# Kernel tuning notes

Hardware: AMD Instinct MI355X
Metric: run time of the kernel (lower is better)

Reference implementation:

```python
import jax, jax.numpy as jnp
import numpy as np
from jax import lax

LEAK = 0.2   # LeakyReLU negative slope
EPS = 1e-5   # LayerNorm eps (torch default)
K = 16       # nsample

def _lrelu(x):
    return jnp.where(x > 0, x, LEAK * x)

def _ln(x, g, b):
    m = x.mean(-1, keepdims=True)
    v = x.var(-1, keepdims=True)
    return (x - m) / jnp.sqrt(v + EPS) * g + b

def _pointconv(xyz, new_xyz, feats, W, b):
    # xyz [B,N,3], new_xyz [B,M,3], feats [B,N,C] -> [B,M,O]
    d2 = (jnp.sum(new_xyz**2, -1)[:, :, None]
          + jnp.sum(xyz**2, -1)[:, None, :]
          - 2.0 * jnp.einsum('bmd,bnd->bmn', new_xyz, xyz))   # [B,M,N]
    _, idx = lax.top_k(-d2, K)                                # kNN indices [B,M,K]
    bidx = jnp.arange(xyz.shape[0])[:, None, None]
    g_xyz = xyz[bidx, idx] - new_xyz[:, :, None, :]           # relative coords [B,M,K,3]
    g_f = feats[bidx, idx]                                    # neighbor feats  [B,M,K,C]
    g = jnp.concatenate([g_xyz, g_f], -1)                     # [B,M,K,C+3]
    h = _lrelu(jnp.einsum('bmkc,co->bmko', g, W) + b)         # local MLP
    return h.max(2)                                           # max-pool over neighbors

def setup_inputs():
    key = jax.random.key(0)
    ks = jax.random.split(key, 8)
    B, N, base, C1 = 256, 1024, 16, 32
    def w(k, shape, fan):
        return jax.random.normal(k, shape, jnp.float32) * (1.0 / np.sqrt(fan))
    return dict(
        point_cloud=jax.random.normal(ks[0], (B, 3, N), jnp.float32),
        pw_W0=w(ks[1], (3, base), 3), pw_b0=jnp.zeros(base), pw_g0=jnp.ones(base), pw_beta0=jnp.zeros(base),
        pw_W1=w(ks[2], (base, base), base), pw_b1=jnp.zeros(base), pw_g1=jnp.ones(base), pw_beta1=jnp.zeros(base),
        pc0_W=w(ks[3], (base + 3, C1), base + 3), pc0_b=jnp.zeros(C1),
        bn_Ws=w(ks[4], (C1, C1 // 4), C1), bn_bs=jnp.zeros(C1 // 4),
        bn_Wc=w(ks[5], (C1 // 4 + 3, 128), C1 // 4 + 3), bn_bc=jnp.zeros(128),
        bn_We=w(ks[6], (128, 256), 128), bn_be=jnp.zeros(256),
    )

def reference(point_cloud, pw_W0, pw_b0, pw_g0, pw_beta0, pw_W1, pw_b1, pw_g1, pw_beta1,
              pc0_W, pc0_b, bn_Ws, bn_bs, bn_Wc, bn_bc, bn_We, bn_be):
    xyz0 = jnp.swapaxes(point_cloud, 1, 2)   # [B,1024,3]
    xyz1 = xyz0[:, ::2]                      # strided downsample -> [B,512,3]
    xyz2 = xyz1[:, ::4]                      # -> [B,128,3]
    # pointwise MLP (Linear-LN-LeakyReLU x2)
    f = _lrelu(_ln(xyz0 @ pw_W0 + pw_b0, pw_g0, pw_beta0))
    f = _lrelu(_ln(f @ pw_W1 + pw_b1, pw_g1, pw_beta1))       # [B,1024,16]
    # PointConv layer 0: 1024 -> 512 points, 16 -> 32 ch
    f = _pointconv(xyz0, xyz1, f, pc0_W, pc0_b)               # [B,512,32]
    # BottleneckStridedPointConv: squeeze (32->8), grouped conv (->128), expand (->256)
    fs = _lrelu(f @ bn_Ws + bn_bs)                            # [B,512,8]
    f = _pointconv(xyz1, xyz2, fs, bn_Wc, bn_bc)              # [B,128,128]
    f = f @ bn_We + bn_be                                     # [B,128,256]
    return f.mean(1)                                          # mean over points -> [B,256]
```

## Files before the change

kernel.cpp:

```cpp
#include <hip/hip_runtime.h>
#include <float.h>
#include <math.h>

#define LEAK 0.2f
#define EPS 1e-5f

__device__ __forceinline__ float lrelu(float v){ return v > 0.f ? v : LEAK*v; }

__device__ __forceinline__ void ln_lrelu16(float* h, const float* __restrict__ g, const float* __restrict__ be){
  float mu = 0.f;
#pragma unroll
  for (int o=0;o<16;o++) mu += h[o];
  mu *= 0.0625f;
  float var = 0.f;
#pragma unroll
  for (int o=0;o<16;o++){ float d = h[o]-mu; var += d*d; }
  var *= 0.0625f;
  float rs = 1.0f / sqrtf(var + EPS);
#pragma unroll
  for (int o=0;o<16;o++){ float v = (h[o]-mu)*rs*g[o] + be[o]; h[o] = lrelu(v); }
}

__global__ __launch_bounds__(256) void prep_kernel(const float* __restrict__ pc,
    const float* __restrict__ W0, const float* __restrict__ b0, const float* __restrict__ g0, const float* __restrict__ be0,
    const float* __restrict__ W1, const float* __restrict__ b1, const float* __restrict__ g1, const float* __restrict__ be1,
    float4* __restrict__ cand, float* __restrict__ feats)
{
  const int p = blockIdx.x*256 + threadIdx.x;
  const int b = p >> 10, n = p & 1023;
  const float* base = pc + b*3072;
  const float x = base[n], y = base[1024+n], z = base[2048+n];
  cand[p] = make_float4(x, y, z, x*x + y*y + z*z);
  float h[16];
#pragma unroll
  for (int o=0;o<16;o++) h[o] = b0[o] + x*W0[o] + y*W0[16+o] + z*W0[32+o];
  ln_lrelu16(h, g0, be0);
  float h2[16];
#pragma unroll
  for (int o=0;o<16;o++){
    float s = b1[o];
#pragma unroll
    for (int c=0;c<16;c++) s += h[c]*W1[c*16+o];
    h2[o] = s;
  }
  ln_lrelu16(h2, g1, be1);
  float4* fo = (float4*)(feats + p*16);
  fo[0] = make_float4(h2[0],h2[1],h2[2],h2[3]);
  fo[1] = make_float4(h2[4],h2[5],h2[6],h2[7]);
  fo[2] = make_float4(h2[8],h2[9],h2[10],h2[11]);
  fo[3] = make_float4(h2[12],h2[13],h2[14],h2[15]);
}

#define KNN_SENT 0xFF7FFC00u
__device__ __forceinline__ unsigned enc_key(float d, int n){
  unsigned u = __float_as_uint(d);
  u ^= (unsigned)(((int)u) >> 31) | 0x80000000u;
  return (u & ~1023u) | (unsigned)n;
}
__device__ __forceinline__ float dec_key(unsigned k){
  unsigned u = k ^ ((unsigned)(~(((int)k) >> 31)) | 0x80000000u);
  return __uint_as_float(u);
}

__device__ __forceinline__ unsigned med3u(unsigned a, unsigned b, unsigned c){
  unsigned d;
  asm("v_med3_u32 %0, %1, %2, %3" : "=v"(d) : "v"(a), "v"(b), "v"(c));
  return d;
}

__device__ __forceinline__ void ins_sorted(unsigned (&dk)[16], unsigned key){
#pragma unroll
  for (int j=15;j>0;--j) dk[j] = med3u(dk[j-1], dk[j], key);
  dk[0] = key < dk[0] ? key : dk[0];
}

template<int QS, int CS, int NQTOT, int NQ, int SPLIT, int NCAND>
__device__ __forceinline__ void knn_body(unsigned* md, float4* scand,
    const float4* __restrict__ cand, int bid, int* __restrict__ idx_out)
{
  constexpr int NC = NCAND / SPLIT;
  constexpr int QG = NQTOT / NQ;
  constexpr int W  = SPLIT*NQ;
  constexpr int QSL = QS / CS;
  const int b = bid / QG, qg = bid % QG;
  const int tid = threadIdx.x;
  const int m = tid & (NQ-1), s = tid / NQ;
  const int mg = qg*NQ + m;
  const float4* __restrict__ cb = cand + b*1024;

  for (int i = tid; i < NCAND; i += NQ*SPLIT)
    scand[i] = cb[i*CS];
  __syncthreads();

  const float4 qv = scand[mg*QSL];
  const float qx2=-2.f*qv.x, qy2=-2.f*qv.y, qz2=-2.f*qv.z;
  const int n0u = __builtin_amdgcn_readfirstlane(s*NC);

  unsigned dk[16];
#pragma unroll
  for (int j=0;j<16;j++) dk[j] = KNN_SENT;

#pragma unroll 8
  for (int t=0;t<32;t++){
    float4 c = scand[n0u+t];
    float d = fmaf(c.x,qx2, fmaf(c.y,qy2, fmaf(c.z,qz2, c.w)));
    ins_sorted(dk, enc_key(d, n0u+t));
  }
  float Tf = dec_key(dk[15]);

  {
    unsigned m32 = 0u;
#pragma unroll 8
    for (int t=32;t<64;t++){
      float4 c = scand[n0u+t];
      float d = fmaf(c.x,qx2, fmaf(c.y,qy2, fmaf(c.z,qz2, c.w)));
      if (d < Tf) m32 |= (1u<<(t-32));
    }
    while (m32){
      const int t = __builtin_ctz(m32) + 32;
      m32 &= m32-1u;
      float4 c = scand[n0u+t];
      float d = fmaf(c.x,qx2, fmaf(c.y,qy2, fmaf(c.z,qz2, c.w)));
      ins_sorted(dk, enc_key(d, n0u+t));
    }
    Tf = dec_key(dk[15]);
  }

  for (int ch=1; ch<NC/64; ch++){
    const int cb0u = n0u + ch*64;
    unsigned long long msk = 0ull;
#pragma unroll 16
    for (int t=0;t<64;t++){
      float4 c = scand[cb0u+t];
      float d = fmaf(c.x,qx2, fmaf(c.y,qy2, fmaf(c.z,qz2, c.w)));
      if (d < Tf) msk |= (1ull<<t);
    }
    while (msk){
      const int t = __builtin_ctzll(msk);
      msk &= msk-1ull;
      float4 c = scand[cb0u+t];
      float d = fmaf(c.x,qx2, fmaf(c.y,qy2, fmaf(c.z,qz2, c.w)));
      ins_sorted(dk, enc_key(d, cb0u+t));
    }
    Tf = dec_key(dk[15]);
  }

  if constexpr (SPLIT > 1){
    if (s > 0){
      const int col = s*NQ + m;
#pragma unroll
      for (int j=0;j<16;j++) md[j*W + col] = dk[j];
    }
#pragma unroll
    for (int step = SPLIT/2; step > 1; step >>= 1){
      __syncthreads();
      if (s < step){
        const int col2 = (s+step)*NQ + m;
#pragma unroll
        for (int j=0;j<16;j++) ins_sorted(dk, md[j*W + col2]);
        if (s > 0){
          const int col = s*NQ + m;
#pragma unroll
          for (int j=0;j<16;j++) md[j*W + col] = dk[j];
        }
      }
    }
    __syncthreads();
    if (s != 0) return;
    const int col2 = NQ + m;
#pragma unroll
    for (int j=0;j<16;j++){
      unsigned o = md[(15-j)*W + col2];
      dk[j] = o < dk[j] ? o : dk[j];
    }
  }

  int ik[16];
#pragma unroll
  for (int j=0;j<16;j++) ik[j] = (int)(dk[j] & 1023u);
  int4* op = (int4*)(idx_out + (b*NQTOT + mg)*16);
  op[0] = make_int4(ik[0],ik[1],ik[2],ik[3]);
  op[1] = make_int4(ik[4],ik[5],ik[6],ik[7]);
  op[2] = make_int4(ik[8],ik[9],ik[10],ik[11]);
  op[3] = make_int4(ik[12],ik[13],ik[14],ik[15]);
}

__global__ __attribute__((amdgpu_flat_work_group_size(1024,1024), amdgpu_waves_per_eu(4,8)))
void knn_fused_kernel(const float4* __restrict__ cand,
                      int* __restrict__ idx1, int* __restrict__ idx2)
{
  __shared__ __align__(16) char smem[81920];
  unsigned* md = (unsigned*)smem;
  if (blockIdx.x < 256){
    float4* scand = (float4*)(smem + 65536);
    knn_body<2,1,512,512,2,1024>(md, scand, cand, blockIdx.x, idx1);
  } else {
    float4* scand = (float4*)(smem + 65536);
    knn_body<8,2,128,128,8,512>(md, scand, cand, blockIdx.x - 256, idx2);
  }
}

__global__ __attribute__((amdgpu_flat_work_group_size(512,512), amdgpu_waves_per_eu(4,4)))
void feat1_kernel(const float4* __restrict__ cand,
    const float* __restrict__ feats, const int* __restrict__ idx1,
    const float* __restrict__ W, const float* __restrict__ Wb,
    const float* __restrict__ Ws,
    float* __restrict__ p1part)
{
  __shared__ float sPT[16*1024];
  const int bx = blockIdx.x;
  const int b = bx >> 1, ob = bx & 1;
  const int ob16 = ob*16;
  const int tid = threadIdx.x;
  const float4* __restrict__ cb = cand + b*1024;
  const float4* __restrict__ fb4 = (const float4*)(feats + b*16384);

#pragma unroll
  for (int i=0;i<2;i++){
    const int j = tid + i*512;
    float4 cj = cb[j];
    float4 f0 = fb4[j*4+0], f1 = fb4[j*4+1], f2 = fb4[j*4+2], f3 = fb4[j*4+3];
    float f[16] = {f0.x,f0.y,f0.z,f0.w, f1.x,f1.y,f1.z,f1.w,
                   f2.x,f2.y,f2.z,f2.w, f3.x,f3.y,f3.z,f3.w};
#pragma unroll
    for (int o4=0;o4<4;o4++){
      float4 s = *(const float4*)(Wb + ob16 + o4*4);
      { float4 wa = *(const float4*)(W +       ob16 + o4*4);
        float4 wb = *(const float4*)(W + 32  + ob16 + o4*4);
        float4 wc = *(const float4*)(W + 64  + ob16 + o4*4);
        s.x = fmaf(cj.x,wa.x, fmaf(cj.y,wb.x, fmaf(cj.z,wc.x, s.x)));
        s.y = fmaf(cj.x,wa.y, fmaf(cj.y,wb.y, fmaf(cj.z,wc.y, s.y)));
        s.z = fmaf(cj.x,wa.z, fmaf(cj.y,wb.z, fmaf(cj.z,wc.z, s.z)));
        s.w = fmaf(cj.x,wa.w, fmaf(cj.y,wb.w, fmaf(cj.z,wc.w, s.w))); }
#pragma unroll
      for (int c=0;c<16;c++){
        float4 w = *(const float4*)(W + (3+c)*32 + ob16 + o4*4);
        s.x = fmaf(f[c], w.x, s.x);
        s.y = fmaf(f[c], w.y, s.y);
        s.z = fmaf(f[c], w.z, s.z);
        s.w = fmaf(f[c], w.w, s.w);
      }
      sPT[(o4*4+0)*1024 + j] = s.x;
      sPT[(o4*4+1)*1024 + j] = s.y;
      sPT[(o4*4+2)*1024 + j] = s.z;
      sPT[(o4*4+3)*1024 + j] = s.w;
    }
  }
  __syncthreads();

  const int m = tid;
  const float4 qv = cb[2*m];
  float Q[16];
#pragma unroll
  for (int i=0;i<4;i++){
    float4 a = *(const float4*)(W +       ob16 + i*4);
    float4 bb= *(const float4*)(W + 32  + ob16 + i*4);
    float4 cc= *(const float4*)(W + 64  + ob16 + i*4);
    Q[i*4+0] = fmaf(qv.x,a.x, fmaf(qv.y,bb.x, qv.z*cc.x));
    Q[i*4+1] = fmaf(qv.x,a.y, fmaf(qv.y,bb.y, qv.z*cc.y));
    Q[i*4+2] = fmaf(qv.x,a.z, fmaf(qv.y,bb.z, qv.z*cc.z));
    Q[i*4+3] = fmaf(qv.x,a.w, fmaf(qv.y,bb.w, qv.z*cc.w));
  }
  int idxr[16];
  { const int4* ip = (const int4*)(idx1 + (b*512+m)*16);
    int4 a=ip[0], b2=ip[1], c2=ip[2], d2=ip[3];
    idxr[0]=a.x; idxr[1]=a.y; idxr[2]=a.z; idxr[3]=a.w;
    idxr[4]=b2.x; idxr[5]=b2.y; idxr[6]=b2.z; idxr[7]=b2.w;
    idxr[8]=c2.x; idxr[9]=c2.y; idxr[10]=c2.z; idxr[11]=c2.w;
    idxr[12]=d2.x; idxr[13]=d2.y; idxr[14]=d2.z; idxr[15]=d2.w; }

  float acc[16];
#pragma unroll
  for (int o=0;o<16;o++) acc[o] = -FLT_MAX;

#pragma unroll 4
  for (int k=0;k<16;k++){
    const int j = idxr[k];
    const float* pj = sPT + j;
#pragma unroll
    for (int o=0;o<16;o++)
      acc[o] = fmaxf(acc[o], pj[o*1024] - Q[o]);
  }

  float fsacc[8] = {0.f,0.f,0.f,0.f,0.f,0.f,0.f,0.f};
#pragma unroll
  for (int o=0;o<16;o++){
    const float a = fmaxf(acc[o], 0.2f*acc[o]);
    float4 u = *(const float4*)(Ws + (ob16+o)*8);
    float4 v = *(const float4*)(Ws + (ob16+o)*8 + 4);
    fsacc[0] = fmaf(a, u.x, fsacc[0]);
    fsacc[1] = fmaf(a, u.y, fsacc[1]);
    fsacc[2] = fmaf(a, u.z, fsacc[2]);
    fsacc[3] = fmaf(a, u.w, fsacc[3]);
    fsacc[4] = fmaf(a, v.x, fsacc[4]);
    fsacc[5] = fmaf(a, v.y, fsacc[5]);
    fsacc[6] = fmaf(a, v.z, fsacc[6]);
    fsacc[7] = fmaf(a, v.w, fsacc[7]);
  }
  float4* op = (float4*)(p1part + ((b*2+ob)*512 + m)*8);
  op[0] = make_float4(fsacc[0],fsacc[1],fsacc[2],fsacc[3]);
  op[1] = make_float4(fsacc[4],fsacc[5],fsacc[6],fsacc[7]);
}

__global__ __attribute__((amdgpu_flat_work_group_size(512,512), amdgpu_waves_per_eu(4,4)))
void feat2_kernel(const float4* __restrict__ cand,
    const float* __restrict__ p1part, const int* __restrict__ idx2,
    const float* __restrict__ Wc, const float* __restrict__ bc,
    const float* __restrict__ bs,
    float* __restrict__ p2red)
{
  __shared__ float sP2[512*32];
  __shared__ float sred[32];
  const int bx = blockIdx.x;
  const int b = bx >> 2, ob = bx & 3;
  const int o_base = ob*32;
  const int tid = threadIdx.x;
  const float4* __restrict__ cb = cand + b*1024;
  if (tid < 32) sred[tid] = 0.f;

  { const float4* __restrict__ pa4 = (const float4*)(p1part + ((b*2+0)*512 + tid)*8);
    const float4* __restrict__ pb4 = (const float4*)(p1part + ((b*2+1)*512 + tid)*8);
    float4 a0 = pa4[0], a1 = pa4[1], c0 = pb4[0], c1 = pb4[1];
    float4 s0 = *(const float4*)(bs), s1 = *(const float4*)(bs+4);
    float f[8];
    f[0]=lrelu(a0.x+c0.x+s0.x); f[1]=lrelu(a0.y+c0.y+s0.y);
    f[2]=lrelu(a0.z+c0.z+s0.z); f[3]=lrelu(a0.w+c0.w+s0.w);
    f[4]=lrelu(a1.x+c1.x+s1.x); f[5]=lrelu(a1.y+c1.y+s1.y);
    f[6]=lrelu(a1.z+c1.z+s1.z); f[7]=lrelu(a1.w+c1.w+s1.w);
    float4 cj = cb[2*tid];
    float* row = sP2 + tid*32;
    const int sw = (tid & 7);
#pragma unroll
    for (int o4=0;o4<8;o4++){
      float4 s = *(const float4*)(bc + o_base + o4*4);
      { float4 wa = *(const float4*)(Wc +        o_base + o4*4);
        float4 wb = *(const float4*)(Wc + 128  + o_base + o4*4);
        float4 wc = *(const float4*)(Wc + 256  + o_base + o4*4);
        s.x = fmaf(cj.x,wa.x, fmaf(cj.y,wb.x, fmaf(cj.z,wc.x, s.x)));
        s.y = fmaf(cj.x,wa.y, fmaf(cj.y,wb.y, fmaf(cj.z,wc.y, s.y)));
        s.z = fmaf(cj.x,wa.z, fmaf(cj.y,wb.z, fmaf(cj.z,wc.z, s.z)));
        s.w = fmaf(cj.x,wa.w, fmaf(cj.y,wb.w, fmaf(cj.z,wc.w, s.w))); }
#pragma unroll
      for (int c=0;c<8;c++){
        float4 w = *(const float4*)(Wc + (3+c)*128 + o_base + o4*4);
        s.x = fmaf(f[c], w.x, s.x);
        s.y = fmaf(f[c], w.y, s.y);
        s.z = fmaf(f[c], w.z, s.z);
        s.w = fmaf(f[c], w.w, s.w);
      }
      *(float4*)(row + ((o4 ^ sw) << 2)) = s;
    }
  }
  __syncthreads();

  const int m = tid >> 2, oq = tid & 3;
  const float4 qv = cb[8*m];
  float Q[8];
  { const int og = o_base + oq*8;
#pragma unroll
    for (int i=0;i<2;i++){
      float4 a = *(const float4*)(Wc +        og + i*4);
      float4 bb= *(const float4*)(Wc + 128  + og + i*4);
      float4 cc= *(const float4*)(Wc + 256  + og + i*4);
      Q[i*4+0] = fmaf(qv.x,a.x, fmaf(qv.y,bb.x, qv.z*cc.x));
      Q[i*4+1] = fmaf(qv.x,a.y, fmaf(qv.y,bb.y, qv.z*cc.y));
      Q[i*4+2] = fmaf(qv.x,a.z, fmaf(qv.y,bb.z, qv.z*cc.z));
      Q[i*4+3] = fmaf(qv.x,a.w, fmaf(qv.y,bb.w, qv.z*cc.w));
    } }
  int idxr[16];
  { const int4* ip = (const int4*)(idx2 + (b*128+m)*16);
    int4 a=ip[0], b2=ip[1], c2=ip[2], d2=ip[3];
    idxr[0]=a.x; idxr[1]=a.y; idxr[2]=a.z; idxr[3]=a.w;
    idxr[4]=b2.x; idxr[5]=b2.y; idxr[6]=b2.z; idxr[7]=b2.w;
    idxr[8]=c2.x; idxr[9]=c2.y; idxr[10]=c2.z; idxr[11]=c2.w;
    idxr[12]=d2.x; idxr[13]=d2.y; idxr[14]=d2.z; idxr[15]=d2.w; }

  float acc[8];
#pragma unroll
  for (int o=0;o<8;o++) acc[o] = -FLT_MAX;

#pragma unroll 4
  for (int k=0;k<16;k++){
    const int j = idxr[k];
    const float* row = sP2 + j*32;
    const int sw = (j & 7);
    float4 p0 = *(const float4*)(row + (((2*oq  ) ^ sw) << 2));
    float4 p1 = *(const float4*)(row + (((2*oq+1) ^ sw) << 2));
    acc[0] = fmaxf(acc[0], p0.x - Q[0]);
    acc[1] = fmaxf(acc[1], p0.y - Q[1]);
    acc[2] = fmaxf(acc[2], p0.z - Q[2]);
    acc[3] = fmaxf(acc[3], p0.w - Q[3]);
    acc[4] = fmaxf(acc[4], p1.x - Q[4]);
    acc[5] = fmaxf(acc[5], p1.y - Q[5]);
    acc[6] = fmaxf(acc[6], p1.z - Q[6]);
    acc[7] = fmaxf(acc[7], p1.w - Q[7]);
  }

#pragma unroll
  for (int o=0;o<8;o++){
    float v = fmaxf(acc[o], 0.2f*acc[o]);
    v += __shfl_xor(v, 4);
    v += __shfl_xor(v, 8);
    v += __shfl_xor(v, 16);
    v += __shfl_xor(v, 32);
    if ((threadIdx.x & 60) == 0)
      atomicAdd(&sred[oq*8+o], v);
  }
  __syncthreads();
  if (tid < 32) p2red[b*128 + o_base + tid] = sred[tid];
}

__global__ __launch_bounds__(256) void final_kernel(const float* __restrict__ p2red,
    const float* __restrict__ We, const float* __restrict__ beF, float* __restrict__ out)
{
  const int b = blockIdx.x, o = threadIdx.x;
  const float* __restrict__ r0 = p2red + b*128;
  float s = 0.f;
#pragma unroll 8
  for (int c=0;c<128;c++) s += r0[c]*We[c*256+o];
  out[b*256+o] = beF[o] + s*0.0078125f;
}

extern "C" void kernel_launch(void* const* d_in, const int* in_sizes, int n_in,
                              void* d_out, int out_size, void* d_ws, size_t ws_size,
                              hipStream_t stream) {
  (void)in_sizes; (void)n_in; (void)out_size; (void)ws_size;
  const float* pc   = (const float*)d_in[0];
  const float* W0   = (const float*)d_in[1];
  const float* b0   = (const float*)d_in[2];
  const float* g0   = (const float*)d_in[3];
  const float* be0  = (const float*)d_in[4];
  const float* W1   = (const float*)d_in[5];
  const float* b1   = (const float*)d_in[6];
  const float* g1   = (const float*)d_in[7];
  const float* be1  = (const float*)d_in[8];
  const float* pcW  = (const float*)d_in[9];
  const float* pcb  = (const float*)d_in[10];
  const float* Ws   = (const float*)d_in[11];
  const float* bs   = (const float*)d_in[12];
  const float* Wc   = (const float*)d_in[13];
  const float* bc   = (const float*)d_in[14];
  const float* We   = (const float*)d_in[15];
  const float* beF  = (const float*)d_in[16];

  char* ws = (char*)d_ws;
  float4* cand0 = (float4*)ws;
  float*  feats = (float*)(ws + (4u<<20));
  float*  p2red = (float*)(ws + (4u<<20));
  int*    idx1  = (int*)  (ws + (20u<<20));
  int*    idx2  = (int*)  (ws + (28u<<20));
  float*  p1part= (float*)(ws + (30u<<20));
  float*  out   = (float*)d_out;

  prep_kernel<<<1024, 256, 0, stream>>>(pc, W0,b0,g0,be0, W1,b1,g1,be1, cand0, feats);
  knn_fused_kernel<<<512, 1024, 0, stream>>>(cand0, idx1, idx2);
  feat1_kernel<<<512, 512, 0, stream>>>(cand0, feats, idx1, pcW, pcb, Ws, p1part);
  feat2_kernel<<<1024, 512, 0, stream>>>(cand0, p1part, idx2, Wc, bc, bs, p2red);
  final_kernel<<<256, 256, 0, stream>>>(p2red, We, beF, out);
}
```

Before: 211.8 us.

## Fold prep into kNN/feat1 and final GEMV into feat2 via last-block counter

Removes the separate prep kernel. kNN now builds its candidate float4s straight from the raw point cloud, and feat1 recomputes the pointwise MLP and LayerNorm per point instead of reading a stored feature buffer. The final expand-and-mean GEMV moves into feat2, where the last of the four blocks per batch, found through an atomic counter, does the work. This cuts two kernel launches and the cand/feats global round-trips, at the cost of redundant MLP compute in feat1 (done by both output-half blocks), a memset, and release/acquire atomics.

```diff
diff --git a/kernel.cpp b/kernel.cpp
--- a/kernel.cpp
+++ b/kernel.cpp
@@ -19,36 +19,6 @@
   float rs = 1.0f / sqrtf(var + EPS);
 #pragma unroll
   for (int o=0;o<16;o++){ float v = (h[o]-mu)*rs*g[o] + be[o]; h[o] = lrelu(v); }
-}
-
-__global__ __launch_bounds__(256) void prep_kernel(const float* __restrict__ pc,
-    const float* __restrict__ W0, const float* __restrict__ b0, const float* __restrict__ g0, const float* __restrict__ be0,
-    const float* __restrict__ W1, const float* __restrict__ b1, const float* __restrict__ g1, const float* __restrict__ be1,
-    float4* __restrict__ cand, float* __restrict__ feats)
-{
-  const int p = blockIdx.x*256 + threadIdx.x;
-  const int b = p >> 10, n = p & 1023;
-  const float* base = pc + b*3072;
-  const float x = base[n], y = base[1024+n], z = base[2048+n];
-  cand[p] = make_float4(x, y, z, x*x + y*y + z*z);
-  float h[16];
-#pragma unroll
-  for (int o=0;o<16;o++) h[o] = b0[o] + x*W0[o] + y*W0[16+o] + z*W0[32+o];
-  ln_lrelu16(h, g0, be0);
-  float h2[16];
-#pragma unroll
-  for (int o=0;o<16;o++){
-    float s = b1[o];
-#pragma unroll
-    for (int c=0;c<16;c++) s += h[c]*W1[c*16+o];
-    h2[o] = s;
-  }
-  ln_lrelu16(h2, g1, be1);
-  float4* fo = (float4*)(feats + p*16);
-  fo[0] = make_float4(h2[0],h2[1],h2[2],h2[3]);
-  fo[1] = make_float4(h2[4],h2[5],h2[6],h2[7]);
-  fo[2] = make_float4(h2[8],h2[9],h2[10],h2[11]);
-  fo[3] = make_float4(h2[12],h2[13],h2[14],h2[15]);
 }
 
 #define KNN_SENT 0xFF7FFC00u
@@ -76,7 +46,7 @@
 
 template<int QS, int CS, int NQTOT, int NQ, int SPLIT, int NCAND>
 __device__ __forceinline__ void knn_body(unsigned* md, float4* scand,
-    const float4* __restrict__ cand, int bid, int* __restrict__ idx_out)
+    const float* __restrict__ pc, int bid, int* __restrict__ idx_out)
 {
   constexpr int NC = NCAND / SPLIT;
   constexpr int QG = NQTOT / NQ;
@@ -86,10 +56,13 @@
   const int tid = threadIdx.x;
   const int m = tid & (NQ-1), s = tid / NQ;
   const int mg = qg*NQ + m;
-  const float4* __restrict__ cb = cand + b*1024;
-
-  for (int i = tid; i < NCAND; i += NQ*SPLIT)
-    scand[i] = cb[i*CS];
+  const float* __restrict__ pcb = pc + b*3072;
+
+  for (int i = tid; i < NCAND; i += NQ*SPLIT){
+    const int n = i*CS;
+    const float x = pcb[n], y = pcb[1024+n], z = pcb[2048+n];
+    scand[i] = make_float4(x, y, z, fmaf(x,x, fmaf(y,y, z*z)));
+  }
   __syncthreads();
 
   const float4 qv = scand[mg*QSL];
@@ -186,23 +159,24 @@
 }
 
 __global__ __attribute__((amdgpu_flat_work_group_size(1024,1024), amdgpu_waves_per_eu(4,8)))
-void knn_fused_kernel(const float4* __restrict__ cand,
+void knn_fused_kernel(const float* __restrict__ pc,
                       int* __restrict__ idx1, int* __restrict__ idx2)
 {
   __shared__ __align__(16) char smem[81920];
   unsigned* md = (unsigned*)smem;
   if (blockIdx.x < 256){
     float4* scand = (float4*)(smem + 65536);
-    knn_body<2,1,512,512,2,1024>(md, scand, cand, blockIdx.x, idx1);
+    knn_body<2,1,512,512,2,1024>(md, scand, pc, blockIdx.x, idx1);
   } else {
     float4* scand = (float4*)(smem + 65536);
-    knn_body<8,2,128,128,8,512>(md, scand, cand, blockIdx.x - 256, idx2);
+    knn_body<8,2,128,128,8,512>(md, scand, pc, blockIdx.x - 256, idx2);
   }
 }
 
 __global__ __attribute__((amdgpu_flat_work_group_size(512,512), amdgpu_waves_per_eu(4,4)))
-void feat1_kernel(const float4* __restrict__ cand,
-    const float* __restrict__ feats, const int* __restrict__ idx1,
+void feat1_kernel(const float* __restrict__ pc, const int* __restrict__ idx1,
+    const float* __restrict__ W0, const float* __restrict__ b0, const float* __restrict__ g0, const float* __restrict__ be0,
+    const float* __restrict__ W1, const float* __restrict__ b1, const float* __restrict__ g1, const float* __restrict__ be1,
     const float* __restrict__ W, const float* __restrict__ Wb,
     const float* __restrict__ Ws,
     float* __restrict__ p1part)
@@ -212,26 +186,35 @@
   const int b = bx >> 1, ob = bx & 1;
   const int ob16 = ob*16;
   const int tid = threadIdx.x;
-  const float4* __restrict__ cb = cand + b*1024;
-  const float4* __restrict__ fb4 = (const float4*)(feats + b*16384);
+  const float* __restrict__ pb = pc + b*3072;
 
 #pragma unroll
   for (int i=0;i<2;i++){
     const int j = tid + i*512;
-    float4 cj = cb[j];
-    float4 f0 = fb4[j*4+0], f1 = fb4[j*4+1], f2 = fb4[j*4+2], f3 = fb4[j*4+3];
-    float f[16] = {f0.x,f0.y,f0.z,f0.w, f1.x,f1.y,f1.z,f1.w,
-                   f2.x,f2.y,f2.z,f2.w, f3.x,f3.y,f3.z,f3.w};
+    const float x = pb[j], y = pb[1024+j], z = pb[2048+j];
+    float h[16];
+#pragma unroll
+    for (int o=0;o<16;o++) h[o] = b0[o] + x*W0[o] + y*W0[16+o] + z*W0[32+o];
+    ln_lrelu16(h, g0, be0);
+    float f[16];
+#pragma unroll
+    for (int o=0;o<16;o++){
+      float s = b1[o];
+#pragma unroll
+      for (int c=0;c<16;c++) s += h[c]*W1[c*16+o];
+      f[o] = s;
+    }
+    ln_lrelu16(f, g1, be1);
 #pragma unroll
     for (int o4=0;o4<4;o4++){
       float4 s = *(const float4*)(Wb + ob16 + o4*4);
       { float4 wa = *(const float4*)(W +       ob16 + o4*4);
         float4 wb = *(const float4*)(W + 32  + ob16 + o4*4);
         float4 wc = *(const float4*)(W + 64  + ob16 + o4*4);
-        s.x = fmaf(cj.x,wa.x, fmaf(cj.y,wb.x, fmaf(cj.z,wc.x, s.x)));
-        s.y = fmaf(cj.x,wa.y, fmaf(cj.y,wb.y, fmaf(cj.z,wc.y, s.y)));
-        s.z = fmaf(cj.x,wa.z, fmaf(cj.y,wb.z, fmaf(cj.z,wc.z, s.z)));
-        s.w = fmaf(cj.x,wa.w, fmaf(cj.y,wb.w, fmaf(cj.z,wc.w, s.w))); }
+        s.x = fmaf(x,wa.x, fmaf(y,wb.x, fmaf(z,wc.x, s.x)));
+        s.y = fmaf(x,wa.y, fmaf(y,wb.y, fmaf(z,wc.y, s.y)));
+        s.z = fmaf(x,wa.z, fmaf(y,wb.z, fmaf(z,wc.z, s.z)));
+        s.w = fmaf(x,wa.w, fmaf(y,wb.w, fmaf(z,wc.w, s.w))); }
 #pragma unroll
       for (int c=0;c<16;c++){
         float4 w = *(const float4*)(W + (3+c)*32 + ob16 + o4*4);
@@ -249,17 +232,17 @@
   __syncthreads();
 
   const int m = tid;
-  const float4 qv = cb[2*m];
+  const float qx = pb[2*m], qy = pb[1024+2*m], qz = pb[2048+2*m];
   float Q[16];
 #pragma unroll
   for (int i=0;i<4;i++){
     float4 a = *(const float4*)(W +       ob16 + i*4);
     float4 bb= *(const float4*)(W + 32  + ob16 + i*4);
     float4 cc= *(const float4*)(W + 64  + ob16 + i*4);
-    Q[i*4+0] = fmaf(qv.x,a.x, fmaf(qv.y,bb.x, qv.z*cc.x));
-    Q[i*4+1] = fmaf(qv.x,a.y, fmaf(qv.y,bb.y, qv.z*cc.y));
-    Q[i*4+2] = fmaf(qv.x,a.z, fmaf(qv.y,bb.z, qv.z*cc.z));
-    Q[i*4+3] = fmaf(qv.x,a.w, fmaf(qv.y,bb.w, qv.z*cc.w));
+    Q[i*4+0] = fmaf(qx,a.x, fmaf(qy,bb.x, qz*cc.x));
+    Q[i*4+1] = fmaf(qx,a.y, fmaf(qy,bb.y, qz*cc.y));
+    Q[i*4+2] = fmaf(qx,a.z, fmaf(qy,bb.z, qz*cc.z));
+    Q[i*4+3] = fmaf(qx,a.w, fmaf(qy,bb.w, qz*cc.w));
   }
   int idxr[16];
   { const int4* ip = (const int4*)(idx1 + (b*512+m)*16);
@@ -303,19 +286,23 @@
 }
 
 __global__ __attribute__((amdgpu_flat_work_group_size(512,512), amdgpu_waves_per_eu(4,4)))
-void feat2_kernel(const float4* __restrict__ cand,
+void feat2_kernel(const float* __restrict__ pc,
     const float* __restrict__ p1part, const int* __restrict__ idx2,
     const float* __restrict__ Wc, const float* __restrict__ bc,
     const float* __restrict__ bs,
-    float* __restrict__ p2red)
+    const float* __restrict__ We, const float* __restrict__ beF,
+    float* __restrict__ p2red, unsigned int* __restrict__ cnt,
+    float* __restrict__ out)
 {
   __shared__ float sP2[512*32];
   __shared__ float sred[32];
+  __shared__ float sfin[128];
+  __shared__ int sLast;
   const int bx = blockIdx.x;
   const int b = bx >> 2, ob = bx & 3;
   const int o_base = ob*32;
   const int tid = threadIdx.x;
-  const float4* __restrict__ cb = cand + b*1024;
+  const float* __restrict__ pb = pc + b*3072;
   if (tid < 32) sred[tid] = 0.f;
 
   { const float4* __restrict__ pa4 = (const float4*)(p1part + ((b*2+0)*512 + tid)*8);
@@ -327,7 +314,7 @@
     f[2]=lrelu(a0.z+c0.z+s0.z); f[3]=lrelu(a0.w+c0.w+s0.w);
     f[4]=lrelu(a1.x+c1.x+s1.x); f[5]=lrelu(a1.y+c1.y+s1.y);
     f[6]=lrelu(a1.z+c1.z+s1.z); f[7]=lrelu(a1.w+c1.w+s1.w);
-    float4 cj = cb[2*tid];
+    const float cjx = pb[2*tid], cjy = pb[1024+2*tid], cjz = pb[2048+2*tid];
     float* row = sP2 + tid*32;
     const int sw = (tid & 7);
 #pragma unroll
@@ -336,10 +323,10 @@
       { float4 wa = *(const float4*)(Wc +        o_base + o4*4);
         float4 wb = *(const float4*)(Wc + 128  + o_base + o4*4);
         float4 wc = *(const float4*)(Wc + 256  + o_base + o4*4);
-        s.x = fmaf(cj.x,wa.x, fmaf(cj.y,wb.x, fmaf(cj.z,wc.x, s.x)));
-        s.y = fmaf(cj.x,wa.y, fmaf(cj.y,wb.y, fmaf(cj.z,wc.y, s.y)));
-        s.z = fmaf(cj.x,wa.z, fmaf(cj.y,wb.z, fmaf(cj.z,wc.z, s.z)));
-        s.w = fmaf(cj.x,wa.w, fmaf(cj.y,wb.w, fmaf(cj.z,wc.w, s.w))); }
+        s.x = fmaf(cjx,wa.x, fmaf(cjy,wb.x, fmaf(cjz,wc.x, s.x)));
+        s.y = fmaf(cjx,wa.y, fmaf(cjy,wb.y, fmaf(cjz,wc.y, s.y)));
+        s.z = fmaf(cjx,wa.z, fmaf(cjy,wb.z, fmaf(cjz,wc.z, s.z)));
+        s.w = fmaf(cjx,wa.w, fmaf(cjy,wb.w, fmaf(cjz,wc.w, s.w))); }
 #pragma unroll
       for (int c=0;c<8;c++){
         float4 w = *(const float4*)(Wc + (3+c)*128 + o_base + o4*4);
@@ -354,7 +341,7 @@
   __syncthreads();
 
   const int m = tid >> 2, oq = tid & 3;
-  const float4 qv = cb[8*m];
+  const float qx = pb[8*m], qy = pb[1024+8*m], qz = pb[2048+8*m];
   float Q[8];
   { const int og = o_base + oq*8;
 #pragma unroll
@@ -362,10 +349,10 @@
       float4 a = *(const float4*)(Wc +        og + i*4);
       float4 bb= *(const float4*)(Wc + 128  + og + i*4);
       float4 cc= *(const float4*)(Wc + 256  + og + i*4);
-      Q[i*4+0] = fmaf(qv.x,a.x, fmaf(qv.y,bb.x, qv.z*cc.x));
-      Q[i*4+1] = fmaf(qv.x,a.y, fmaf(qv.y,bb.y, qv.z*cc.y));
-      Q[i*4+2] = fmaf(qv.x,a.z, fmaf(qv.y,bb.z, qv.z*cc.z));
-      Q[i*4+3] = fmaf(qv.x,a.w, fmaf(qv.y,bb.w, qv.z*cc.w));
+      Q[i*4+0] = fmaf(qx,a.x, fmaf(qy,bb.x, qz*cc.x));
+      Q[i*4+1] = fmaf(qx,a.y, fmaf(qy,bb.y, qz*cc.y));
+      Q[i*4+2] = fmaf(qx,a.z, fmaf(qy,bb.z, qz*cc.z));
+      Q[i*4+3] = fmaf(qx,a.w, fmaf(qy,bb.w, qz*cc.w));
     } }
   int idxr[16];
   { const int4* ip = (const int4*)(idx2 + (b*128+m)*16);
@@ -407,18 +394,29 @@
       atomicAdd(&sred[oq*8+o], v);
   }
   __syncthreads();
-  if (tid < 32) p2red[b*128 + o_base + tid] = sred[tid];
-}
-
-__global__ __launch_bounds__(256) void final_kernel(const float* __restrict__ p2red,
-    const float* __restrict__ We, const float* __restrict__ beF, float* __restrict__ out)
-{
-  const int b = blockIdx.x, o = threadIdx.x;
-  const float* __restrict__ r0 = p2red + b*128;
-  float s = 0.f;
+
+  if (tid < 32)
+    __hip_atomic_store(&p2red[b*128 + o_base + tid], sred[tid],
+                       __ATOMIC_RELEASE, __HIP_MEMORY_SCOPE_AGENT);
+  __syncthreads();
+  if (tid == 0){
+    unsigned old = __hip_atomic_fetch_add(&cnt[b], 1u,
+                       __ATOMIC_ACQ_REL, __HIP_MEMORY_SCOPE_AGENT);
+    sLast = (old == 3u) ? 1 : 0;
+  }
+  __syncthreads();
+  if (sLast){
+    if (tid < 128)
+      sfin[tid] = __hip_atomic_load(&p2red[b*128 + tid],
+                       __ATOMIC_ACQUIRE, __HIP_MEMORY_SCOPE_AGENT);
+    __syncthreads();
+    if (tid < 256){
+      float s = 0.f;
 #pragma unroll 8
-  for (int c=0;c<128;c++) s += r0[c]*We[c*256+o];
-  out[b*256+o] = beF[o] + s*0.0078125f;
+      for (int c=0;c<128;c++) s += sfin[c]*We[c*256+tid];
+      out[b*256+tid] = beF[tid] + s*0.0078125f;
+    }
+  }
 }
 
 extern "C" void kernel_launch(void* const* d_in, const int* in_sizes, int n_in,
@@ -442,19 +440,21 @@
   const float* bc   = (const float*)d_in[14];
   const float* We   = (const float*)d_in[15];
   const float* beF  = (const float*)d_in[16];
+  (void)pcb;
 
   char* ws = (char*)d_ws;
-  float4* cand0 = (float4*)ws;
-  float*  feats = (float*)(ws + (4u<<20));
-  float*  p2red = (float*)(ws + (4u<<20));
-  int*    idx1  = (int*)  (ws + (20u<<20));
-  int*    idx2  = (int*)  (ws + (28u<<20));
-  float*  p1part= (float*)(ws + (30u<<20));
+  int*    idx1  = (int*)  ws;
+  int*    idx2  = (int*)  (ws + (8u<<20));
+  float*  p1part= (float*)(ws + (10u<<20));
+  float*  p2red = (float*)(ws + (18u<<20));
+  unsigned int* cnt = (unsigned int*)(ws + (19u<<20));
   float*  out   = (float*)d_out;
 
-  prep_kernel<<<1024, 256, 0, stream>>>(pc, W0,b0,g0,be0, W1,b1,g1,be1, cand0, feats);
-  knn_fused_kernel<<<512, 1024, 0, stream>>>(cand0, idx1, idx2);
-  feat1_kernel<<<512, 512, 0, stream>>>(cand0, feats, idx1, pcW, pcb, Ws, p1part);
-  feat2_kernel<<<1024, 512, 0, stream>>>(cand0, p1part, idx2, Wc, bc, bs, p2red);
-  final_kernel<<<256, 256, 0, stream>>>(p2red, We, beF, out);
-}
+  hipMemsetAsync(cnt, 0, 256*sizeof(unsigned int), stream);
+
+  knn_fused_kernel<<<512, 1024, 0, stream>>>(pc, idx1, idx2);
+  feat1_kernel<<<512, 512, 0, stream>>>(pc, idx1, W0,b0,g0,be0, W1,b1,g1,be1,
+                                        pcW, pcb, Ws, p1part);
+  feat2_kernel<<<1024, 512, 0, stream>>>(pc, p1part, idx2, Wc, bc, bs,
+                                         We, beF, p2red, cnt, out);
+}
```

Result: slower. 254.6 us (+20.2%).
